# Optimization experiments

Measured on AMD Instinct MI355X. Metric: run time of the kernel, lower is better.

## Reference

```python
import jax, jax.numpy as jnp
import numpy as np
import math

B, A, T = 64, 23, 128          # batch, num_agents, max seq len
D, AE, S, H = 256, 32, 6, 8    # d_model, agent_encoding_dim, static_dim, heads
DK = D // H                     # 32
DM = D + AE                     # 288, MHA q/k/v dim
NEG = -1e10                     # masked_fill constant from source


def sinusoidal_pe(pos, d):
    # pos: int array [...], returns [..., d] standard transformer PE at positions pos
    half = jnp.arange(d // 2, dtype=jnp.float32)
    div = jnp.exp(-half * (math.log(10000.0) * 2.0 / d))          # [d/2]
    ang = pos[..., None].astype(jnp.float32) * div                # [..., d/2]
    return jnp.stack([jnp.sin(ang), jnp.cos(ang)], axis=-1).reshape(*pos.shape, d)


def setup_inputs() -> dict:
    key = jax.random.key(0)
    ks = jax.random.split(key, 20)
    std = 0.02
    data = jax.random.normal(ks[0], (B, A, T), jnp.float32)
    lengths = jax.random.randint(ks[1], (B, A), 0, T + 1).astype(jnp.int32)   # mask arg = lengths
    t = jnp.arange(T, dtype=jnp.int32)
    time = jnp.where(t[None, None, :] < lengths[:, :, None], t[None, None, :], -1)  # [B,A,T], -1 = pad
    static = jax.random.normal(ks[2], (B, S), jnp.float32)
    # per-agent Linear(1, D): weight [A, D], bias [A, D]
    W_embed = std * jax.random.normal(ks[3], (A, D), jnp.float32)
    b_embed = std * jax.random.normal(ks[4], (A, D), jnp.float32)
    E_var = std * jax.random.normal(ks[5], (A, AE), jnp.float32)            # VariateEncoding table
    W_static = std * jax.random.normal(ks[6], (S, D), jnp.float32)
    b_static = jnp.zeros((D,), jnp.float32)
    Wq = std * jax.random.normal(ks[7], (DM, D), jnp.float32); bq = jnp.zeros((D,), jnp.float32)
    Wk = std * jax.random.normal(ks[8], (DM, D), jnp.float32); bk = jnp.zeros((D,), jnp.float32)
    Wv = std * jax.random.normal(ks[9], (DM, D), jnp.float32); bv = jnp.zeros((D,), jnp.float32)
    Wo = std * jax.random.normal(ks[10], (D, DM), jnp.float32); bo = jnp.zeros((DM,), jnp.float32)
    Wg = std * jax.random.normal(ks[11], (DM + D, 1), jnp.float32); bg = jnp.zeros((1,), jnp.float32)
    return dict(data=data, time=time, mask=lengths, static=static,
                W_embed=W_embed, b_embed=b_embed, E_var=E_var,
                W_static=W_static, b_static=b_static,
                Wq=Wq, bq=bq, Wk=Wk, bk=bk, Wv=Wv, bv=bv, Wo=Wo, bo=bo,
                Wg=Wg, bg=bg)


def reference(data, time, mask, static, W_embed, b_embed, E_var, W_static, b_static,
              Wq, bq, Wk, bk, Wv, bv, Wo, bo, Wg, bg):
    lengths = mask                                            # [B,A] sequence lengths
    t = jnp.arange(T)
    valid = t[None, None, :] < lengths[:, :, None]            # [B,A,T] bool
    # mask_matrix[i,:len,:len]=1 double loop -> vectorized outer product
    mask4 = valid[:, :, :, None] & valid[:, :, None, :]       # [B,A,T,T]

    # per-agent Linear(1, D) loop -> batched rank-1 affine, then ReLU
    data_embeds = jax.nn.relu(data[..., None] * W_embed[None, :, None, :]
                              + b_embed[None, :, None, :])    # [B,A,T,D]

    # src_pe: sinusoidal positional encoding at (clamped) time values
    pe = sinusoidal_pe(jnp.maximum(time, 0), D)               # [B,A,T,D]
    src = data_embeds + pe

    # variate (agent-id) embedding concat -> [B,A,T,D+AE]; encoder = identity
    var = jnp.broadcast_to(E_var[None, :, None, :], (B, A, T, AE))
    memory = jnp.concatenate([src, var], axis=-1)             # [B,A,T,DM]

    # time-masked mean pool over T
    time_mask = time >= 0                                     # [B,A,T]
    memory = jnp.where(time_mask[..., None], memory, 0.0)
    counts = time_mask.sum(axis=2).astype(memory.dtype)       # [B,A]
    agentwise = memory.sum(axis=2) / (counts[..., None] + 1e-9)  # [B,A,DM]

    # custom MHA (dim='Time'): q_len = 1 per agent, keys/values over T
    q = jnp.einsum('bae,ed->bad', agentwise, Wq) + bq          # [B,A,D]
    k = jnp.einsum('bate,ed->batd', memory, Wk) + bk           # [B,A,T,D]
    v = jnp.einsum('bate,ed->batd', memory, Wv) + bv
    qh = q.reshape(B, A, H, DK)                                # [B,A,H,DK] (q_len=1 squeezed)
    kh = k.reshape(B, A, T, H, DK).transpose(0, 1, 3, 2, 4)    # [B,A,H,T,DK]
    vh = v.reshape(B, A, T, H, DK).transpose(0, 1, 3, 2, 4)
    scores = jnp.einsum('bahd,bahtd->baht', qh, kh) / math.sqrt(DK)  # [B,A,H,T]
    amask = mask4[:, :, 0, :]                                  # [B,A,T] row 0 of per-agent mask
    scores = jnp.where(amask[:, :, None, :], scores, NEG)
    p = jax.nn.softmax(scores, axis=-1)                        # dropout = eval (identity)
    ctx = jnp.einsum('baht,bahtd->bahd', p, vh).reshape(B, A, D)
    agent_feat = jnp.einsum('bad,de->bae', ctx, Wo) + bo       # [B,A,DM]

    # agent-masked mean pool over agents
    agent_mask = counts > 0                                    # [B,A]
    agent_feat = jnp.where(agent_mask[..., None], agent_feat, 0.0)
    denom = agent_mask.sum(axis=1).astype(agent_feat.dtype) + 1e-9
    aggre = agent_feat.sum(axis=1) / denom[:, None]            # [B,DM]

    static_feat = static @ W_static + b_static                 # [B,D]
    all_feature = jnp.concatenate([aggre, static_feat], axis=-1)  # [B,DM+D]
    return all_feature @ Wg + bg                               # [B,1]


if __name__ == '__main__':
    out = reference(**setup_inputs())
    print(out.shape, jnp.asarray(out).dtype)
```

## Files before the change

### kernel.cpp

```cpp
#include <hip/hip_runtime.h>
#include <math.h>

#define NB 64
#define NA 23
#define NT 128
#define ND 256
#define NAE 32
#define NS 6
#define NH 8
#define NDM 288

#define OFF_PET    0
#define OFF_PECUM  32768
#define OFF_WKT    65792
#define OFF_VWO    131328
#define OFF_CST    133632
#define OFF_S      133648

__global__ __launch_bounds__(256) void setup_kernel(
    const float* __restrict__ Wk, const float* __restrict__ Wv,
    const float* __restrict__ Wo, const float* __restrict__ Wg,
    const float* __restrict__ bv, const float* __restrict__ bo,
    const float* __restrict__ W_static, const float* __restrict__ b_static,
    const float* __restrict__ bg, float* __restrict__ ws)
{
    const int blk = blockIdx.x;
    const int tid = threadIdx.x;
    float* peT   = ws + OFF_PET;
    float* PEcum = ws + OFF_PECUM;
    float* WkT   = ws + OFF_WKT;
    float* VWo   = ws + OFF_VWO;
    float* cst   = ws + OFF_CST;

    if (blk < 128) {
        const int g = tid >> 7, t = tid & 127;
        const int e = blk * 2 + g;
        const int i = e >> 1;
        const float kdiv = 0.07195578415606394f;
        const float dv = expf(-(float)i * kdiv);
        const float ang = (float)t * dv;
        const float v = (e & 1) ? cosf(ang) : sinf(ang);
        peT[e * NT + t] = v;
        __shared__ float buf[256];
        buf[tid] = v;
        #pragma unroll
        for (int s = 1; s < 128; s <<= 1) {
            __syncthreads();
            float add = (t >= s) ? buf[tid - s] : 0.f;
            __syncthreads();
            buf[tid] += add;
        }
        __syncthreads();
        PEcum[(t + 1) * ND + e] = buf[tid];
    } else if (blk < 384) {
        const int j = blk - 128;
        const float scale = 0.17677669529663687f;
        WkT[j * 256 + tid] = Wk[tid * ND + j] * scale;
    } else if (blk < 392) {
        const int h = blk - 384;
        __shared__ float wog[32];
        {
            const int jj = tid >> 3, sub = tid & 7;
            const int j = h * 32 + jj;
            float acc = 0.f;
            const int m0 = sub * 36;
            #pragma unroll 4
            for (int m = m0; m < m0 + 36; ++m)
                acc = fmaf(Wo[j * NDM + m], Wg[m], acc);
            acc += __shfl_down(acc, 4, 8);
            acc += __shfl_down(acc, 2, 8);
            acc += __shfl_down(acc, 1, 8);
            if (sub == 0) wog[jj] = acc;
        }
        __syncthreads();
        for (int e = tid; e < NDM; e += 256) {
            float acc = 0.f;
            #pragma unroll 8
            for (int jj = 0; jj < 32; ++jj)
                acc = fmaf(Wv[e * ND + h * 32 + jj], wog[jj], acc);
            VWo[h * NDM + e] = acc;
        }
        if (tid == 0) {
            float acc = 0.f;
            #pragma unroll 8
            for (int jj = 0; jj < 32; ++jj)
                acc = fmaf(bv[h * 32 + jj], wog[jj], acc);
            cst[8 + h] = acc;
        }
    } else {
        const int i = tid >> 5, sub = tid & 31;
        float acc = 0.f;
        if (i < 6) {
            for (int m = sub; m < 256; m += 32)
                acc = fmaf(W_static[i * ND + m], Wg[NDM + m], acc);
        } else if (i == 6) {
            for (int m = sub; m < 256; m += 32)
                acc = fmaf(b_static[m], Wg[NDM + m], acc);
        } else {
            for (int m = sub; m < NDM; m += 32)
                acc = fmaf(bo[m], Wg[m], acc);
        }
        #pragma unroll
        for (int off = 16; off > 0; off >>= 1)
            acc += __shfl_down(acc, off, 32);
        if (sub == 0) cst[i] = (i == 6) ? acc + bg[0] : acc;
    }
}

__global__ __launch_bounds__(256) void main_kernel(
    const float* __restrict__ data, const int* __restrict__ lengths,
    const float* __restrict__ W_embed, const float* __restrict__ b_embed,
    const float* __restrict__ E_var,
    const float* __restrict__ Wq, const float* __restrict__ bq,
    float* __restrict__ ws)
{
    const int wg = blockIdx.x;
    const int a = wg % NA;
    const int tid = threadIdx.x;
    const int L = lengths[wg];

    if (L == 0) {
        if (tid == 0) ws[OFF_S + wg] = 0.f;
        return;
    }

    __shared__ float xs[NT];
    __shared__ float agentwise[NDM];
    __shared__ float qs[ND];
    __shared__ float2 Wb[ND];
    __shared__ __align__(16) float combo[ND * 16];
    __shared__ float evvS[NH];
    __shared__ float red[4];

    const float* peT   = ws + OFF_PET;
    const float* PEcum = ws + OFF_PECUM;
    const float* WkT   = ws + OFF_WKT;
    const float* VWo   = ws + OFF_VWO;
    const float* cstp  = ws + OFF_CST;

    if (tid < NT) xs[tid] = data[wg * NT + tid];
    __syncthreads();
    {
        const int e = tid;
        const float We = W_embed[a * ND + e];
        const float be = b_embed[a * ND + e];
        Wb[e] = make_float2(We, be);
        float acc = 0.f;
        #pragma unroll 4
        for (int t = 0; t < L; ++t)
            acc += fmaxf(fmaf(xs[t], We, be), 0.f);
        agentwise[e] = (acc + PEcum[L * ND + e]) / (float)L;
    }
    if (tid < NAE) agentwise[ND + tid] = E_var[a * NAE + tid];
    __syncthreads();

    {
        const int j = tid;
        float acc = bq[j];
        #pragma unroll 4
        for (int f = 0; f < NDM; ++f)
            acc = fmaf(agentwise[f], Wq[f * ND + j], acc);
        qs[j] = acc;
    }
    __syncthreads();

    {
        const int h = tid >> 5, eo = tid & 31;
        const float* wr = WkT + (h * 32) * 256;
        for (int eb = 0; eb < 8; ++eb) {
            const int e = eb * 32 + eo;
            float acc = 0.f;
            #pragma unroll 8
            for (int j = 0; j < 32; ++j)
                acc = fmaf(wr[j * 256 + e], qs[h * 32 + j], acc);
            combo[e * 16 + h] = acc;
        }
    }
    for (int idx = tid; idx < NH * ND; idx += 256) {
        const int h = idx >> 8, e = idx & 255;
        combo[e * 16 + 8 + h] = VWo[h * NDM + e];
    }
    {
        const int h = tid >> 5, ee = tid & 31;
        float v = E_var[a * NAE + ee] * VWo[h * NDM + ND + ee];
        v += __shfl_down(v, 16, 32);
        v += __shfl_down(v, 8, 32);
        v += __shfl_down(v, 4, 32);
        v += __shfl_down(v, 2, 32);
        v += __shfl_down(v, 1, 32);
        if (ee == 0) evvS[h] = v;
    }
    __syncthreads();

    {
        const int t = tid & 127;
        const int half = tid >> 7;
        const float xt = xs[t];
        float accS[8], accM[8];
        #pragma unroll
        for (int h = 0; h < 8; ++h) { accS[h] = 0.f; accM[h] = 0.f; }
        const int ebase = half * 128;
        const float4* comboV = (const float4*)combo + ebase * 4;
        const float* peCol = peT + ebase * NT + t;
        #pragma unroll 2
        for (int ee = 0; ee < 128; ++ee) {
            const float2 wb = Wb[ebase + ee];
            const float m = fmaxf(fmaf(xt, wb.x, wb.y), 0.f) + peCol[ee * NT];
            const float4 c0 = comboV[ee * 4 + 0];
            const float4 c1 = comboV[ee * 4 + 1];
            const float4 c2 = comboV[ee * 4 + 2];
            const float4 c3 = comboV[ee * 4 + 3];
            accS[0] = fmaf(m, c0.x, accS[0]);
            accS[1] = fmaf(m, c0.y, accS[1]);
            accS[2] = fmaf(m, c0.z, accS[2]);
            accS[3] = fmaf(m, c0.w, accS[3]);
            accS[4] = fmaf(m, c1.x, accS[4]);
            accS[5] = fmaf(m, c1.y, accS[5]);
            accS[6] = fmaf(m, c1.z, accS[6]);
            accS[7] = fmaf(m, c1.w, accS[7]);
            accM[0] = fmaf(m, c2.x, accM[0]);
            accM[1] = fmaf(m, c2.y, accM[1]);
            accM[2] = fmaf(m, c2.z, accM[2]);
            accM[3] = fmaf(m, c2.w, accM[3]);
            accM[4] = fmaf(m, c3.x, accM[4]);
            accM[5] = fmaf(m, c3.y, accM[5]);
            accM[6] = fmaf(m, c3.z, accM[6]);
            accM[7] = fmaf(m, c3.w, accM[7]);
        }
        __syncthreads();
        float* sc   = combo;
        float* mvb  = combo + 1024;
        float* scP1 = combo + 2048;
        float* mvP1 = combo + 3072;
        if (half == 1) {
            #pragma unroll
            for (int h = 0; h < 8; ++h) {
                scP1[h * NT + t] = accS[h];
                mvP1[h * NT + t] = accM[h];
            }
        }
        __syncthreads();
        if (half == 0) {
            #pragma unroll
            for (int h = 0; h < 8; ++h) {
                sc[h * NT + t]  = accS[h] + scP1[h * NT + t];
                mvb[h * NT + t] = accM[h] + mvP1[h * NT + t];
            }
        }
    }
    __syncthreads();

    {
        const float* sc  = combo;
        const float* mvb = combo + 1024;
        const int wv = tid >> 6, lane = tid & 63;
        float wsum = 0.f;
        for (int hh = 0; hh < 2; ++hh) {
            const int h = wv * 2 + hh;
            float s1 = (lane < L) ? sc[h * NT + lane] : -3e38f;
            float s2 = (lane + 64 < L) ? sc[h * NT + 64 + lane] : -3e38f;
            float mx = fmaxf(s1, s2);
            #pragma unroll
            for (int off = 32; off > 0; off >>= 1)
                mx = fmaxf(mx, __shfl_down(mx, off, 64));
            mx = __shfl(mx, 0, 64);
            const float vbv = evvS[h] + cstp[8 + h];
            float e1 = (lane < L) ? __expf(s1 - mx) : 0.f;
            float e2 = (lane + 64 < L) ? __expf(s2 - mx) : 0.f;
            float num = e1 * (mvb[h * NT + lane] + vbv);
            num = fmaf(e2, mvb[h * NT + 64 + lane] + vbv, num);
            float den = e1 + e2;
            #pragma unroll
            for (int off = 32; off > 0; off >>= 1) {
                num += __shfl_down(num, off, 64);
                den += __shfl_down(den, off, 64);
            }
            if (lane == 0) wsum += num / den;
        }
        if (lane == 0) red[wv] = wsum;
    }
    __syncthreads();
    if (tid == 0) {
        ws[OFF_S + wg] = cstp[7] + red[0] + red[1] + red[2] + red[3];
    }
}

__global__ __launch_bounds__(64) void final_kernel(
    const float* __restrict__ statics, const int* __restrict__ lengths,
    const float* __restrict__ ws, float* __restrict__ out)
{
    const int b = threadIdx.x;
    const float* s_arr = ws + OFF_S;
    const float* cst = ws + OFF_CST;
    float sum = 0.f;
    int n = 0;
    for (int a = 0; a < NA; ++a) {
        if (lengths[b * NA + a] > 0) { sum += s_arr[b * NA + a]; ++n; }
    }
    float o = sum / ((float)n + 1e-9f);
    #pragma unroll
    for (int i = 0; i < NS; ++i)
        o = fmaf(statics[b * NS + i], cst[i], o);
    o += cst[6];
    out[b] = o;
}

extern "C" void kernel_launch(void* const* d_in, const int* in_sizes, int n_in,
                              void* d_out, int out_size, void* d_ws, size_t ws_size,
                              hipStream_t stream) {
    const float* data     = (const float*)d_in[0];
    const int*   mask     = (const int*)d_in[2];
    const float* statics  = (const float*)d_in[3];
    const float* W_embed  = (const float*)d_in[4];
    const float* b_embed  = (const float*)d_in[5];
    const float* E_var    = (const float*)d_in[6];
    const float* W_static = (const float*)d_in[7];
    const float* b_static = (const float*)d_in[8];
    const float* Wq       = (const float*)d_in[9];
    const float* bq       = (const float*)d_in[10];
    const float* Wk       = (const float*)d_in[11];
    const float* Wv       = (const float*)d_in[13];
    const float* bv       = (const float*)d_in[14];
    const float* Wo       = (const float*)d_in[15];
    const float* bo       = (const float*)d_in[16];
    const float* Wg       = (const float*)d_in[17];
    const float* bg       = (const float*)d_in[18];
    float* out = (float*)d_out;
    float* ws  = (float*)d_ws;

    setup_kernel<<<dim3(393), dim3(256), 0, stream>>>(Wk, Wv, Wo, Wg, bv, bo,
                                                      W_static, b_static, bg, ws);
    main_kernel<<<dim3(NB * NA), dim3(256), 0, stream>>>(data, mask, W_embed, b_embed,
                                                         E_var, Wq, bq, ws);
    final_kernel<<<dim3(1), dim3(64), 0, stream>>>(statics, mask, ws, out);
}
```

Measured before the change: 165.5 us.

## Remap score/value loop to skip padded timesteps and pad combo stride

Reassigns the main score/value accumulation so each thread covers two timesteps (t and t+64) for four heads instead of one timestep for eight heads. When the sequence length is at most 64, it skips computing the upper half of the timesteps. The combo stride grows from 16 to 20 floats per row, likely to reduce LDS bank conflicts. Two smaller loops get split accumulators to shorten dependency chains, and the E_var load is read from shared memory instead of global memory.

```diff
diff --git a/kernel.cpp b/kernel.cpp
--- a/kernel.cpp
+++ b/kernel.cpp
@@ -128,7 +128,7 @@
     __shared__ float agentwise[NDM];
     __shared__ float qs[ND];
     __shared__ float2 Wb[ND];
-    __shared__ __align__(16) float combo[ND * 16];
+    __shared__ __align__(16) float combo[ND * 20];
     __shared__ float evvS[NH];
     __shared__ float red[4];
 
@@ -145,11 +145,17 @@
         const float We = W_embed[a * ND + e];
         const float be = b_embed[a * ND + e];
         Wb[e] = make_float2(We, be);
-        float acc = 0.f;
-        #pragma unroll 4
-        for (int t = 0; t < L; ++t)
-            acc += fmaxf(fmaf(xs[t], We, be), 0.f);
-        agentwise[e] = (acc + PEcum[L * ND + e]) / (float)L;
+        float s0 = 0.f, s1 = 0.f, s2 = 0.f, s3 = 0.f;
+        int t = 0;
+        for (; t + 4 <= L; t += 4) {
+            s0 += fmaxf(fmaf(xs[t],     We, be), 0.f);
+            s1 += fmaxf(fmaf(xs[t + 1], We, be), 0.f);
+            s2 += fmaxf(fmaf(xs[t + 2], We, be), 0.f);
+            s3 += fmaxf(fmaf(xs[t + 3], We, be), 0.f);
+        }
+        for (; t < L; ++t)
+            s0 += fmaxf(fmaf(xs[t], We, be), 0.f);
+        agentwise[e] = (((s0 + s1) + (s2 + s3)) + PEcum[L * ND + e]) / (float)L;
     }
     if (tid < NAE) agentwise[ND + tid] = E_var[a * NAE + tid];
     __syncthreads();
@@ -167,22 +173,25 @@
     {
         const int h = tid >> 5, eo = tid & 31;
         const float* wr = WkT + (h * 32) * 256;
+        const float* qh = qs + h * 32;
         for (int eb = 0; eb < 8; ++eb) {
             const int e = eb * 32 + eo;
-            float acc = 0.f;
-            #pragma unroll 8
-            for (int j = 0; j < 32; ++j)
-                acc = fmaf(wr[j * 256 + e], qs[h * 32 + j], acc);
-            combo[e * 16 + h] = acc;
+            float acc = 0.f, acc2 = 0.f;
+            #pragma unroll
+            for (int j = 0; j < 32; j += 2) {
+                acc  = fmaf(wr[ j      * 256 + e], qh[j],     acc);
+                acc2 = fmaf(wr[(j + 1) * 256 + e], qh[j + 1], acc2);
+            }
+            combo[e * 20 + h] = acc + acc2;
         }
     }
     for (int idx = tid; idx < NH * ND; idx += 256) {
         const int h = idx >> 8, e = idx & 255;
-        combo[e * 16 + 8 + h] = VWo[h * NDM + e];
+        combo[e * 20 + 8 + h] = VWo[h * NDM + e];
     }
     {
         const int h = tid >> 5, ee = tid & 31;
-        float v = E_var[a * NAE + ee] * VWo[h * NDM + ND + ee];
+        float v = agentwise[ND + ee] * VWo[h * NDM + ND + ee];
         v += __shfl_down(v, 16, 32);
         v += __shfl_down(v, 8, 32);
         v += __shfl_down(v, 4, 32);
@@ -193,58 +202,79 @@
     __syncthreads();
 
     {
-        const int t = tid & 127;
-        const int half = tid >> 7;
-        const float xt = xs[t];
-        float accS[8], accM[8];
+        const int t  = tid & 63;
+        const int hh = (tid >> 6) & 1;
+        const int c  = tid >> 7;
+        const int ebase = c * 128;
+        const float xt1 = xs[t];
+        const float xt2 = xs[t + 64];
+        const float* peCol = peT + ebase * NT + t;
+        const float4* comboV = (const float4*)combo;
+        float aS1[4], aS2[4], aM1[4], aM2[4];
         #pragma unroll
-        for (int h = 0; h < 8; ++h) { accS[h] = 0.f; accM[h] = 0.f; }
-        const int ebase = half * 128;
-        const float4* comboV = (const float4*)combo + ebase * 4;
-        const float* peCol = peT + ebase * NT + t;
-        #pragma unroll 2
-        for (int ee = 0; ee < 128; ++ee) {
-            const float2 wb = Wb[ebase + ee];
-            const float m = fmaxf(fmaf(xt, wb.x, wb.y), 0.f) + peCol[ee * NT];
-            const float4 c0 = comboV[ee * 4 + 0];
-            const float4 c1 = comboV[ee * 4 + 1];
-            const float4 c2 = comboV[ee * 4 + 2];
-            const float4 c3 = comboV[ee * 4 + 3];
-            accS[0] = fmaf(m, c0.x, accS[0]);
-            accS[1] = fmaf(m, c0.y, accS[1]);
-            accS[2] = fmaf(m, c0.z, accS[2]);
-            accS[3] = fmaf(m, c0.w, accS[3]);
-            accS[4] = fmaf(m, c1.x, accS[4]);
-            accS[5] = fmaf(m, c1.y, accS[5]);
-            accS[6] = fmaf(m, c1.z, accS[6]);
-            accS[7] = fmaf(m, c1.w, accS[7]);
-            accM[0] = fmaf(m, c2.x, accM[0]);
-            accM[1] = fmaf(m, c2.y, accM[1]);
-            accM[2] = fmaf(m, c2.z, accM[2]);
-            accM[3] = fmaf(m, c2.w, accM[3]);
-            accM[4] = fmaf(m, c3.x, accM[4]);
-            accM[5] = fmaf(m, c3.y, accM[5]);
-            accM[6] = fmaf(m, c3.z, accM[6]);
-            accM[7] = fmaf(m, c3.w, accM[7]);
+        for (int k = 0; k < 4; ++k) { aS1[k] = 0.f; aS2[k] = 0.f; aM1[k] = 0.f; aM2[k] = 0.f; }
+
+        if (L > 64) {
+            #pragma unroll 2
+            for (int ee = 0; ee < 128; ++ee) {
+                const int e = ebase + ee;
+                const float2 wb = Wb[e];
+                const float pe1 = peCol[ee * NT];
+                const float pe2 = peCol[ee * NT + 64];
+                const float lin1 = fmaf(xt1, wb.x, wb.y);
+                const float lin2 = fmaf(xt2, wb.x, wb.y);
+                const float m1 = fmaxf(lin1, 0.f) + pe1;
+                const float m2 = fmaxf(lin2, 0.f) + pe2;
+                const float4 cq = comboV[e * 5 + hh];
+                const float4 cm = comboV[e * 5 + 2 + hh];
+                aS1[0] = fmaf(m1, cq.x, aS1[0]); aS1[1] = fmaf(m1, cq.y, aS1[1]);
+                aS1[2] = fmaf(m1, cq.z, aS1[2]); aS1[3] = fmaf(m1, cq.w, aS1[3]);
+                aS2[0] = fmaf(m2, cq.x, aS2[0]); aS2[1] = fmaf(m2, cq.y, aS2[1]);
+                aS2[2] = fmaf(m2, cq.z, aS2[2]); aS2[3] = fmaf(m2, cq.w, aS2[3]);
+                aM1[0] = fmaf(m1, cm.x, aM1[0]); aM1[1] = fmaf(m1, cm.y, aM1[1]);
+                aM1[2] = fmaf(m1, cm.z, aM1[2]); aM1[3] = fmaf(m1, cm.w, aM1[3]);
+                aM2[0] = fmaf(m2, cm.x, aM2[0]); aM2[1] = fmaf(m2, cm.y, aM2[1]);
+                aM2[2] = fmaf(m2, cm.z, aM2[2]); aM2[3] = fmaf(m2, cm.w, aM2[3]);
+            }
+        } else {
+            #pragma unroll 2
+            for (int ee = 0; ee < 128; ++ee) {
+                const int e = ebase + ee;
+                const float2 wb = Wb[e];
+                const float pe1 = peCol[ee * NT];
+                const float m1 = fmaxf(fmaf(xt1, wb.x, wb.y), 0.f) + pe1;
+                const float4 cq = comboV[e * 5 + hh];
+                const float4 cm = comboV[e * 5 + 2 + hh];
+                aS1[0] = fmaf(m1, cq.x, aS1[0]); aS1[1] = fmaf(m1, cq.y, aS1[1]);
+                aS1[2] = fmaf(m1, cq.z, aS1[2]); aS1[3] = fmaf(m1, cq.w, aS1[3]);
+                aM1[0] = fmaf(m1, cm.x, aM1[0]); aM1[1] = fmaf(m1, cm.y, aM1[1]);
+                aM1[2] = fmaf(m1, cm.z, aM1[2]); aM1[3] = fmaf(m1, cm.w, aM1[3]);
+            }
         }
         __syncthreads();
-        float* sc   = combo;
-        float* mvb  = combo + 1024;
-        float* scP1 = combo + 2048;
-        float* mvP1 = combo + 3072;
-        if (half == 1) {
-            #pragma unroll
-            for (int h = 0; h < 8; ++h) {
-                scP1[h * NT + t] = accS[h];
-                mvP1[h * NT + t] = accM[h];
+        float* scF = combo;
+        float* mvF = combo + 1024;
+        float* pS  = combo + 2048;
+        float* pM  = combo + 3072;
+        if (c == 1) {
+            #pragma unroll
+            for (int k = 0; k < 4; ++k) {
+                const int h = hh * 4 + k;
+                pS[h * NT + t]      = aS1[k];
+                pS[h * NT + t + 64] = aS2[k];
+                pM[h * NT + t]      = aM1[k];
+                pM[h * NT + t + 64] = aM2[k];
             }
         }
         __syncthreads();
-        if (half == 0) {
-            #pragma unroll
-            for (int h = 0; h < 8; ++h) {
-                sc[h * NT + t]  = accS[h] + scP1[h * NT + t];
-                mvb[h * NT + t] = accM[h] + mvP1[h * NT + t];
+        if (c == 0) {
+            #pragma unroll
+            for (int k = 0; k < 4; ++k) {
+                const int h = hh * 4 + k;
+                scF[h * NT + t]      = aS1[k] + pS[h * NT + t];
+                scF[h * NT + t + 64] = aS2[k] + pS[h * NT + t + 64];
+                mvF[h * NT + t]      = aM1[k] + pM[h * NT + t];
+                mvF[h * NT + t + 64] = aM2[k] + pM[h * NT + t + 64];
             }
         }
     }
@@ -280,9 +310,8 @@
         if (lane == 0) red[wv] = wsum;
     }
     __syncthreads();
-    if (tid == 0) {
+    if (tid == 0)
         ws[OFF_S + wg] = cstp[7] + red[0] + red[1] + red[2] + red[3];
-    }
 }
 
 __global__ __launch_bounds__(64) void final_kernel(
```

New measurement: 174.4 us. +5.4%, slower.
